# Kernel optimization log

Measured on AMD Instinct MI355X. Metric: run time of the kernel, lower is better.

## Reference

```python
import jax, jax.numpy as jnp
import numpy as np

NUM_HEADS = 16  # init kwarg num_attention_heads


def setup_inputs() -> dict:
    key = jax.random.key(0)
    k1, k2, k3, k4 = jax.random.split(key, 4)
    B, T, E = 2, 2048, 1024
    query = jax.random.normal(k1, (B, T, E), dtype=jnp.float32)
    key_t = jax.random.normal(k2, (B, T, E), dtype=jnp.float32)
    value = jax.random.normal(k3, (B, T, E), dtype=jnp.float32)
    # final output projection (nn.Linear(hidden, hidden, bias=False)); torch stores [out,in]
    W_out = jax.random.normal(k4, (E, E), dtype=jnp.float32) * 0.02
    return {"query": query, "key": key_t, "value": value, "W_out": W_out}


def reference(query, key, value, W_out):
    # NOTE: in the source, the per-head q_i/k_i/v_i linear projections are
    # overwritten by reshapes of the raw inputs, so the qs/ks/vs weights are
    # dead code. Every head computes identical output; mean over heads is a
    # no-op. We reproduce that exact math here.
    B, T, E = query.shape
    H = NUM_HEADS
    d = E // H  # head_dim; also d_k used in the 1/sqrt(d_k) scaling

    def split_heads(x):  # [B,T,E] -> [B,H,T,d]
        return x.reshape(B, T, H, d).transpose(0, 2, 1, 3)

    q = split_heads(query)
    k = split_heads(key)
    v = split_heads(value)

    scale = jnp.sqrt(jnp.asarray(d, dtype=jnp.float32))
    scores = jnp.einsum('bhtd,bhsd->bhts', q, k) / scale  # [B,H,T,T]
    attn = jax.nn.softmax(scores, axis=-1)
    head = jnp.einsum('bhts,bhsd->bhtd', attn, v)         # [B,H,T,d]
    head = head.transpose(0, 2, 1, 3).reshape(B, T, E)    # concat heads

    # mean over H identical head outputs == head; final linear (no bias)
    outputs = head @ W_out.T                              # [B,T,E]
    # mean over H identical attention maps == attn, returned as [B*H,T,T]
    attention = attn.reshape(B * H, T, T)
    return outputs, attention
```

## Files before the change

kernel.cpp:

```cpp
#include <hip/hip_runtime.h>
#include <hip/hip_fp16.h>

#define B_NUM  2
#define T_DIM  2048
#define E_DIM  1024
#define H_NUM  16
#define D_HEAD 64
#define BH_NUM (B_NUM * H_NUM)
#define NT     (T_DIM / 64)

using half8  = __attribute__((ext_vector_type(8))) _Float16;
using half4v = __attribute__((ext_vector_type(4))) _Float16;
using f32x4  = __attribute__((ext_vector_type(4))) float;

#define AS1 __attribute__((address_space(1)))
#define AS3 __attribute__((address_space(3)))

#define QSCALE 0.18033688011112042f

#define BAR_VM(N)                                                       \
    do {                                                                \
        asm volatile("s_waitcnt vmcnt(" #N ")" ::: "memory");           \
        __builtin_amdgcn_s_barrier();                                   \
        __builtin_amdgcn_sched_barrier(0);                              \
    } while (0)

__device__ __forceinline__ void bar_plain() {
    __builtin_amdgcn_s_barrier();
    __builtin_amdgcn_sched_barrier(0);
}

__global__ void cast_f16_kernel(const float* __restrict__ in,
                                _Float16* __restrict__ out, int n4) {
    int stride = gridDim.x * blockDim.x;
    for (int i = blockIdx.x * blockDim.x + threadIdx.x; i < n4; i += stride) {
        float4 v = reinterpret_cast<const float4*>(in)[i];
        half4v h;
        h[0] = (_Float16)v.x; h[1] = (_Float16)v.y;
        h[2] = (_Float16)v.z; h[3] = (_Float16)v.w;
        reinterpret_cast<half4v*>(out)[i] = h;
    }
}

__global__ void transpose_v_kernel(const float* __restrict__ V,
                                   _Float16* __restrict__ Vt) {
    __shared__ float tile[64][65];
    int s0 = blockIdx.x * 64;
    int bh = blockIdx.y;
    int b = bh >> 4, h = bh & 15;
    int t = threadIdx.x;

    int row = t >> 2;
    int c0  = (t & 3) * 16;
    const float* src = V + ((size_t)(b * T_DIM + s0 + row)) * E_DIM + h * D_HEAD + c0;
#pragma unroll
    for (int j = 0; j < 16; j += 4) {
        float4 v = *reinterpret_cast<const float4*>(src + j);
        tile[row][c0 + j + 0] = v.x;
        tile[row][c0 + j + 1] = v.y;
        tile[row][c0 + j + 2] = v.z;
        tile[row][c0 + j + 3] = v.w;
    }
    __syncthreads();

    int d  = t >> 2;
    int sc = (t & 3) * 16;
    half8 h0, h1;
#pragma unroll
    for (int j = 0; j < 8; ++j) {
        h0[j] = (_Float16)tile[sc + j][d];
        h1[j] = (_Float16)tile[sc + 8 + j][d];
    }
    _Float16* dst = Vt + ((size_t)(bh * D_HEAD + d)) * T_DIM + s0 + sc;
    *reinterpret_cast<half8*>(dst)     = h0;
    *reinterpret_cast<half8*>(dst + 8) = h1;
}

__device__ __forceinline__ void stage_gl(const _Float16* __restrict__ g,
                                         size_t stride, _Float16* lds,
                                         int w, int lane) {
    int r0 = lane >> 3;
    int c  = (lane & 7) ^ r0;
#pragma unroll
    for (int j = 0; j < 2; ++j) {
        int r = (w + 4 * j) * 8 + r0;
        const _Float16* src = g + (size_t)r * stride + c * 8;
        _Float16* dst = lds + (w + 4 * j) * 512;
        __builtin_amdgcn_global_load_lds((const AS1 void*)src, (AS3 void*)dst,
                                         16, 0, 0);
    }
}

__device__ __forceinline__ half8 read_frag64(const _Float16* lds, int row, int chunk) {
    int csw = chunk ^ (row & 7);
    return *reinterpret_cast<const half8*>(lds + row * 64 + csw * 8);
}

__global__ __launch_bounds__(256) void attn_kernel(
        const float* __restrict__ Q, const _Float16* __restrict__ Kh,
        const _Float16* __restrict__ Vt, float* __restrict__ attn_out,
        _Float16* __restrict__ head_h) {
    __shared__ __align__(16) _Float16 kbuf[2][64 * 64];
    __shared__ __align__(16) _Float16 vbuf[2][64 * 64];
    __shared__ __align__(16) _Float16 pbuf[4][16 * 64];

    int tid  = threadIdx.x;
    int wq   = tid >> 6;
    int lane = tid & 63;
    int l15  = lane & 15;
    int lg   = lane >> 4;

    int flat = blockIdx.x;
    int i    = flat >> 3;
    int bh   = (flat & 7) * 4 + (i >> 4);
    int q0   = (i & 15) * 128;
    int b = bh >> 4, h = bh & 15;

    half8 qfA[2], qfB[2];
#pragma unroll
    for (int half_ = 0; half_ < 2; ++half_) {
        const float* qsrc = Q + ((size_t)(b * T_DIM + q0 + half_ * 64 + wq * 16 + l15)) * E_DIM
                          + h * D_HEAD;
        half8* qf = half_ ? qfB : qfA;
#pragma unroll
        for (int ks = 0; ks < 2; ++ks) {
            float4 a0 = *reinterpret_cast<const float4*>(qsrc + (lg + 4 * ks) * 8);
            float4 a1 = *reinterpret_cast<const float4*>(qsrc + (lg + 4 * ks) * 8 + 4);
            qf[ks][0] = (_Float16)(a0.x * QSCALE); qf[ks][1] = (_Float16)(a0.y * QSCALE);
            qf[ks][2] = (_Float16)(a0.z * QSCALE); qf[ks][3] = (_Float16)(a0.w * QSCALE);
            qf[ks][4] = (_Float16)(a1.x * QSCALE); qf[ks][5] = (_Float16)(a1.y * QSCALE);
            qf[ks][6] = (_Float16)(a1.z * QSCALE); qf[ks][7] = (_Float16)(a1.w * QSCALE);
        }
    }

    const _Float16* kg = Kh + ((size_t)b * T_DIM) * E_DIM + h * D_HEAD;
    const _Float16* vg = Vt + (size_t)bh * D_HEAD * T_DIM;

#define P1TILE(KB, QF, LS)                                                     \
    {                                                                          \
        f32x4 acc[4];                                                          \
        _Pragma("unroll")                                                      \
        for (int ct = 0; ct < 4; ++ct) acc[ct] = (f32x4){0.f, 0.f, 0.f, 0.f};  \
        _Pragma("unroll")                                                      \
        for (int ks = 0; ks < 2; ++ks)                                         \
            _Pragma("unroll")                                                  \
            for (int ct = 0; ct < 4; ++ct) {                                   \
                half8 kf = read_frag64((KB), ct * 16 + l15, lg + 4 * ks);      \
                acc[ct] = __builtin_amdgcn_mfma_f32_16x16x32_f16(              \
                    kf, (QF)[ks], acc[ct], 0, 0, 0);                           \
            }                                                                  \
        _Pragma("unroll")                                                      \
        for (int ct = 0; ct < 4; ++ct)                                         \
            _Pragma("unroll")                                                  \
            for (int r = 0; r < 4; ++r)                                        \
                (LS) += __builtin_amdgcn_exp2f(acc[ct][r]);                    \
    }

#define P2TILE(KB, VB, QF, RL, ABROW, OACC)                                    \
    {                                                                          \
        f32x4 acc[4];                                                          \
        _Pragma("unroll")                                                      \
        for (int ct = 0; ct < 4; ++ct) acc[ct] = (f32x4){0.f, 0.f, 0.f, 0.f};  \
        _Pragma("unroll")                                                      \
        for (int ks = 0; ks < 2; ++ks)                                         \
            _Pragma("unroll")                                                  \
            for (int ct = 0; ct < 4; ++ct) {                                   \
                half8 kf = read_frag64((KB), ct * 16 + l15, lg + 4 * ks);      \
                acc[ct] = __builtin_amdgcn_mfma_f32_16x16x32_f16(              \
                    kf, (QF)[ks], acc[ct], 0, 0, 0);                           \
            }                                                                  \
        _Pragma("unroll")                                                      \
        for (int ct = 0; ct < 4; ++ct) {                                       \
            f32x4 p;                                                           \
            p[0] = __builtin_amdgcn_exp2f(acc[ct][0]) * (RL);                  \
            p[1] = __builtin_amdgcn_exp2f(acc[ct][1]) * (RL);                  \
            p[2] = __builtin_amdgcn_exp2f(acc[ct][2]) * (RL);                  \
            p[3] = __builtin_amdgcn_exp2f(acc[ct][3]) * (RL);                  \
            *reinterpret_cast<f32x4*>((ABROW) + ct * 16) = p;                  \
            half4v ph;                                                         \
            ph[0] = (_Float16)p[0]; ph[1] = (_Float16)p[1];                    \
            ph[2] = (_Float16)p[2]; ph[3] = (_Float16)p[3];                    \
            int cc = (ct * 4 + lg) ^ l15;                                      \
            *reinterpret_cast<half4v*>(pw + l15 * 64 + cc * 4) = ph;           \
        }                                                                      \
    }

#define PVTILE(VB, OACC)                                                       \
    {                                                                          \
        _Pragma("unroll")                                                      \
        for (int ks = 0; ks < 2; ++ks) {                                       \
            int c0 = 2 * (lg + 4 * ks);                                        \
            half4v lo = *reinterpret_cast<const half4v*>(                      \
                pw + l15 * 64 + ((c0)     ^ l15) * 4);                         \
            half4v hi = *reinterpret_cast<const half4v*>(                      \
                pw + l15 * 64 + ((c0 + 1) ^ l15) * 4);                         \
            half8 pa;                                                          \
            pa[0] = lo[0]; pa[1] = lo[1]; pa[2] = lo[2]; pa[3] = lo[3];        \
            pa[4] = hi[0]; pa[5] = hi[1]; pa[6] = hi[2]; pa[7] = hi[3];        \
            _Pragma("unroll")                                                  \
            for (int cd = 0; cd < 4; ++cd) {                                   \
                half8 vf = read_frag64((VB), cd * 16 + l15, lg + 4 * ks);      \
                (OACC)[cd] = __builtin_amdgcn_mfma_f32_16x16x32_f16(           \
                    pa, vf, (OACC)[cd], 0, 0, 0);                              \
            }                                                                  \
        }                                                                      \
    }

    float* ab = attn_out + (size_t)bh * T_DIM * T_DIM;
    _Float16* pw = pbuf[wq];
    int myqA = q0 + wq * 16 + l15;
    int myqB = myqA + 64;

    float lsumA = 0.0f, lsumB = 0.0f;
    int cur = 0;
    stage_gl(kg, E_DIM, kbuf[0], wq, lane);
    for (int t = 0; t < NT - 1; ++t) {
        stage_gl(kg + (size_t)(t + 1) * 64 * E_DIM, E_DIM, kbuf[cur ^ 1], wq, lane);
        BAR_VM(2);
        P1TILE(kbuf[cur], qfA, lsumA);
        bar_plain();
        cur ^= 1;
    }
    BAR_VM(0);
    P1TILE(kbuf[cur], qfA, lsumA);

    lsumA += __shfl_xor(lsumA, 16);
    lsumA += __shfl_xor(lsumA, 32);
    float rlA = 1.0f / lsumA;

    f32x4 oacc[4];
#pragma unroll
    for (int cd = 0; cd < 4; ++cd) oacc[cd] = (f32x4){0.f, 0.f, 0.f, 0.f};

    bar_plain();

    cur = 0;
    stage_gl(kg, E_DIM, kbuf[0], wq, lane);
    stage_gl(vg, T_DIM, vbuf[0], wq, lane);
    for (int t = 0; t < NT; ++t) {
        if (t < NT - 1) {
            stage_gl(kg + (size_t)(t + 1) * 64 * E_DIM, E_DIM, kbuf[cur ^ 1], wq, lane);
            stage_gl(vg + (t + 1) * 64, T_DIM, vbuf[cur ^ 1], wq, lane);
        }
        if (t == 0)           BAR_VM(4);
        else if (t < NT - 1)  BAR_VM(8);
        else                  BAR_VM(4);
        const _Float16* kb = kbuf[cur];
        const _Float16* vb = vbuf[cur];

        float* abrowA = ab + (size_t)myqA * T_DIM + t * 64 + lg * 4;
        P2TILE(kb, vb, qfA, rlA, abrowA, oacc);
        P1TILE(kb, qfB, lsumB);
        PVTILE(vb, oacc);
        bar_plain();
        cur ^= 1;
    }

    lsumB += __shfl_xor(lsumB, 16);
    lsumB += __shfl_xor(lsumB, 32);
    float rlB = 1.0f / lsumB;

    {
        _Float16* hw = head_h + ((size_t)(b * T_DIM + q0 + wq * 16)) * E_DIM + h * D_HEAD;
#pragma unroll
        for (int cd = 0; cd < 4; ++cd)
#pragma unroll
            for (int r = 0; r < 4; ++r)
                hw[(size_t)(lg * 4 + r) * E_DIM + cd * 16 + l15] = (_Float16)oacc[cd][r];
    }

#pragma unroll
    for (int cd = 0; cd < 4; ++cd) oacc[cd] = (f32x4){0.f, 0.f, 0.f, 0.f};

    cur = 0;
    stage_gl(kg, E_DIM, kbuf[0], wq, lane);
    stage_gl(vg, T_DIM, vbuf[0], wq, lane);
    for (int t = 0; t < NT; ++t) {
        if (t < NT - 1) {
            stage_gl(kg + (size_t)(t + 1) * 64 * E_DIM, E_DIM, kbuf[cur ^ 1], wq, lane);
            stage_gl(vg + (t + 1) * 64, T_DIM, vbuf[cur ^ 1], wq, lane);
        }
        if (t == 0)           BAR_VM(4);
        else if (t < NT - 1)  BAR_VM(8);
        else                  BAR_VM(4);
        const _Float16* kb = kbuf[cur];
        const _Float16* vb = vbuf[cur];

        float* abrowB = ab + (size_t)myqB * T_DIM + t * 64 + lg * 4;
        P2TILE(kb, vb, qfB, rlB, abrowB, oacc);
        PVTILE(vb, oacc);
        bar_plain();
        cur ^= 1;
    }

    {
        _Float16* hw = head_h + ((size_t)(b * T_DIM + q0 + 64 + wq * 16)) * E_DIM + h * D_HEAD;
#pragma unroll
        for (int cd = 0; cd < 4; ++cd)
#pragma unroll
            for (int r = 0; r < 4; ++r)
                hw[(size_t)(lg * 4 + r) * E_DIM + cd * 16 + l15] = (_Float16)oacc[cd][r];
    }
#undef P1TILE
#undef P2TILE
#undef PVTILE
}

__global__ __launch_bounds__(256) void proj_kernel(
        const _Float16* __restrict__ A, const _Float16* __restrict__ Wh,
        float* __restrict__ out) {
    __shared__ __align__(16) _Float16 abuf[2][64 * 64];
    __shared__ __align__(16) _Float16 bbuf[2][64 * 64];

    int tid  = threadIdx.x;
    int wq   = tid >> 6;
    int lane = tid & 63;
    int l15  = lane & 15;
    int lg   = lane >> 4;

    int m0 = blockIdx.x * 64;
    int n0 = blockIdx.y * 64;

    f32x4 acc[4];
#pragma unroll
    for (int ct = 0; ct < 4; ++ct) acc[ct] = (f32x4){0.f, 0.f, 0.f, 0.f};

    int cur = 0;
    stage_gl(A  + (size_t)m0 * E_DIM, E_DIM, abuf[0], wq, lane);
    stage_gl(Wh + (size_t)n0 * E_DIM, E_DIM, bbuf[0], wq, lane);
    for (int t = 0; t < E_DIM / 64; ++t) {
        if (t + 1 < E_DIM / 64) {
            stage_gl(A  + (size_t)m0 * E_DIM + (t + 1) * 64, E_DIM, abuf[cur ^ 1], wq, lane);
            stage_gl(Wh + (size_t)n0 * E_DIM + (t + 1) * 64, E_DIM, bbuf[cur ^ 1], wq, lane);
            BAR_VM(4);
        } else {
            BAR_VM(0);
        }
#pragma unroll
        for (int ks = 0; ks < 2; ++ks) {
            half8 hf = read_frag64(abuf[cur], wq * 16 + l15, lg + 4 * ks);
#pragma unroll
            for (int ct = 0; ct < 4; ++ct) {
                half8 wf = read_frag64(bbuf[cur], ct * 16 + l15, lg + 4 * ks);
                acc[ct] = __builtin_amdgcn_mfma_f32_16x16x32_f16(wf, hf, acc[ct], 0, 0, 0);
            }
        }
        bar_plain();
        cur ^= 1;
    }

    float* orow = out + (size_t)(m0 + wq * 16 + l15) * E_DIM + n0 + lg * 4;
#pragma unroll
    for (int ct = 0; ct < 4; ++ct) {
        f32x4 o;
        o[0] = acc[ct][0]; o[1] = acc[ct][1]; o[2] = acc[ct][2]; o[3] = acc[ct][3];
        *reinterpret_cast<f32x4*>(orow + ct * 16) = o;
    }
}

extern "C" void kernel_launch(void* const* d_in, const int* in_sizes, int n_in,
                              void* d_out, int out_size, void* d_ws, size_t ws_size,
                              hipStream_t stream) {
    const float* q = (const float*)d_in[0];
    const float* k = (const float*)d_in[1];
    const float* v = (const float*)d_in[2];
    const float* w = (const float*)d_in[3];

    float* outs = (float*)d_out;
    float* attn = outs + (size_t)B_NUM * T_DIM * E_DIM;

    char* ws = (char*)d_ws;
    _Float16* Kh = (_Float16*)(ws);
    _Float16* Vt = (_Float16*)(ws + (size_t)(8  << 20));
    _Float16* Wh = (_Float16*)(ws + (size_t)(16 << 20));
    _Float16* Hh = (_Float16*)(ws + (size_t)(18 << 20));

    int nqkv4 = B_NUM * T_DIM * E_DIM / 4;
    int nw4   = E_DIM * E_DIM / 4;

    cast_f16_kernel<<<1024, 256, 0, stream>>>(k, Kh, nqkv4);
    cast_f16_kernel<<<512, 256, 0, stream>>>(w, Wh, nw4);
    transpose_v_kernel<<<dim3(T_DIM / 64, BH_NUM), 256, 0, stream>>>(v, Vt);
    attn_kernel<<<(T_DIM / 128) * BH_NUM, 256, 0, stream>>>(q, Kh, Vt, attn, Hh);
    proj_kernel<<<dim3((B_NUM * T_DIM) / 64, E_DIM / 64), 256, 0, stream>>>(Hh, Wh, outs);
}
```

Before: 228.0 us.

## Fuse prep kernels, rotate KV tile order, add MFMA priority and deeper pass-1 prefetch

Merges the K cast, W cast and V transpose into one prep kernel launch to save launch overhead and tail gaps. In the attention kernel, each block starts its KV sweep at a rotated tile offset so that blocks sharing a head hit different K/V tiles at the same moment. The first (row-sum) pass now prefetches two tiles at a time, borrowing vbuf as a second double buffer. The MFMA sections are wrapped in s_setprio to favour matrix issue. Together these aim to cut launch count, cache and channel contention and pipeline stalls, at the cost of more complex indexing.

After: 203.9 us. 1.12x faster.

```diff
diff --git a/kernel.cpp b/kernel.cpp
--- a/kernel.cpp
+++ b/kernel.cpp
@@ -30,50 +30,60 @@
     __builtin_amdgcn_sched_barrier(0);
 }
 
-__global__ void cast_f16_kernel(const float* __restrict__ in,
-                                _Float16* __restrict__ out, int n4) {
-    int stride = gridDim.x * blockDim.x;
-    for (int i = blockIdx.x * blockDim.x + threadIdx.x; i < n4; i += stride) {
-        float4 v = reinterpret_cast<const float4*>(in)[i];
-        half4v h;
-        h[0] = (_Float16)v.x; h[1] = (_Float16)v.y;
-        h[2] = (_Float16)v.z; h[3] = (_Float16)v.w;
-        reinterpret_cast<half4v*>(out)[i] = h;
-    }
-}
-
-__global__ void transpose_v_kernel(const float* __restrict__ V,
-                                   _Float16* __restrict__ Vt) {
+#define TP_BLOCKS  (NT * BH_NUM)
+#define CAST_BLOCKS 1280
+__global__ void prep_kernel(const float* __restrict__ kin,
+                            const float* __restrict__ win,
+                            const float* __restrict__ V,
+                            _Float16* __restrict__ Kh,
+                            _Float16* __restrict__ Wh,
+                            _Float16* __restrict__ Vt,
+                            int nk4, int ntot4) {
     __shared__ float tile[64][65];
-    int s0 = blockIdx.x * 64;
-    int bh = blockIdx.y;
-    int b = bh >> 4, h = bh & 15;
     int t = threadIdx.x;
 
-    int row = t >> 2;
-    int c0  = (t & 3) * 16;
-    const float* src = V + ((size_t)(b * T_DIM + s0 + row)) * E_DIM + h * D_HEAD + c0;
-#pragma unroll
-    for (int j = 0; j < 16; j += 4) {
-        float4 v = *reinterpret_cast<const float4*>(src + j);
-        tile[row][c0 + j + 0] = v.x;
-        tile[row][c0 + j + 1] = v.y;
-        tile[row][c0 + j + 2] = v.z;
-        tile[row][c0 + j + 3] = v.w;
-    }
-    __syncthreads();
-
-    int d  = t >> 2;
-    int sc = (t & 3) * 16;
-    half8 h0, h1;
-#pragma unroll
-    for (int j = 0; j < 8; ++j) {
-        h0[j] = (_Float16)tile[sc + j][d];
-        h1[j] = (_Float16)tile[sc + 8 + j][d];
-    }
-    _Float16* dst = Vt + ((size_t)(bh * D_HEAD + d)) * T_DIM + s0 + sc;
-    *reinterpret_cast<half8*>(dst)     = h0;
-    *reinterpret_cast<half8*>(dst + 8) = h1;
+    if (blockIdx.x < TP_BLOCKS) {
+        int s0 = (blockIdx.x & 31) * 64;
+        int bh = blockIdx.x >> 5;
+        int b = bh >> 4, h = bh & 15;
+
+        int row = t >> 2;
+        int c0  = (t & 3) * 16;
+        const float* src = V + ((size_t)(b * T_DIM + s0 + row)) * E_DIM + h * D_HEAD + c0;
+#pragma unroll
+        for (int j = 0; j < 16; j += 4) {
+            float4 v = *reinterpret_cast<const float4*>(src + j);
+            tile[row][c0 + j + 0] = v.x;
+            tile[row][c0 + j + 1] = v.y;
+            tile[row][c0 + j + 2] = v.z;
+            tile[row][c0 + j + 3] = v.w;
+        }
+        __syncthreads();
+
+        int d  = t >> 2;
+        int sc = (t & 3) * 16;
+        half8 h0, h1;
+#pragma unroll
+        for (int j = 0; j < 8; ++j) {
+            h0[j] = (_Float16)tile[sc + j][d];
+            h1[j] = (_Float16)tile[sc + 8 + j][d];
+        }
+        _Float16* dst = Vt + ((size_t)(bh * D_HEAD + d)) * T_DIM + s0 + sc;
+        *reinterpret_cast<half8*>(dst)     = h0;
+        *reinterpret_cast<half8*>(dst + 8) = h1;
+    } else {
+        int stride = CAST_BLOCKS * 256;
+        for (int i = (blockIdx.x - TP_BLOCKS) * 256 + t; i < ntot4; i += stride) {
+            const float* src = (i < nk4) ? kin : win;
+            _Float16* dst    = (i < nk4) ? Kh  : Wh;
+            int j            = (i < nk4) ? i   : i - nk4;
+            float4 v = reinterpret_cast<const float4*>(src)[j];
+            half4v hh;
+            hh[0] = (_Float16)v.x; hh[1] = (_Float16)v.y;
+            hh[2] = (_Float16)v.z; hh[3] = (_Float16)v.w;
+            reinterpret_cast<half4v*>(dst)[j] = hh;
+        }
+    }
 }
 
 __device__ __forceinline__ void stage_gl(const _Float16* __restrict__ g,
@@ -94,6 +104,18 @@
 __device__ __forceinline__ half8 read_frag64(const _Float16* lds, int row, int chunk) {
     int csw = chunk ^ (row & 7);
     return *reinterpret_cast<const half8*>(lds + row * 64 + csw * 8);
+}
+
+__device__ __forceinline__ void load_qfrag(const float* qsrc, int lg, half8* qf) {
+#pragma unroll
+    for (int ks = 0; ks < 2; ++ks) {
+        float4 a0 = *reinterpret_cast<const float4*>(qsrc + (lg + 4 * ks) * 8);
+        float4 a1 = *reinterpret_cast<const float4*>(qsrc + (lg + 4 * ks) * 8 + 4);
+        qf[ks][0] = (_Float16)(a0.x * QSCALE); qf[ks][1] = (_Float16)(a0.y * QSCALE);
+        qf[ks][2] = (_Float16)(a0.z * QSCALE); qf[ks][3] = (_Float16)(a0.w * QSCALE);
+        qf[ks][4] = (_Float16)(a1.x * QSCALE); qf[ks][5] = (_Float16)(a1.y * QSCALE);
+        qf[ks][6] = (_Float16)(a1.z * QSCALE); qf[ks][7] = (_Float16)(a1.w * QSCALE);
+    }
 }
 
 __global__ __launch_bounds__(256) void attn_kernel(
@@ -113,25 +135,15 @@
     int flat = blockIdx.x;
     int i    = flat >> 3;
     int bh   = (flat & 7) * 4 + (i >> 4);
-    int q0   = (i & 15) * 128;
+    int qt   = i & 15;
+    int q0   = qt * 128;
+    int rot  = i & 31;
+    int rot2 = rot & 30;
     int b = bh >> 4, h = bh & 15;
 
     half8 qfA[2], qfB[2];
-#pragma unroll
-    for (int half_ = 0; half_ < 2; ++half_) {
-        const float* qsrc = Q + ((size_t)(b * T_DIM + q0 + half_ * 64 + wq * 16 + l15)) * E_DIM
-                          + h * D_HEAD;
-        half8* qf = half_ ? qfB : qfA;
-#pragma unroll
-        for (int ks = 0; ks < 2; ++ks) {
-            float4 a0 = *reinterpret_cast<const float4*>(qsrc + (lg + 4 * ks) * 8);
-            float4 a1 = *reinterpret_cast<const float4*>(qsrc + (lg + 4 * ks) * 8 + 4);
-            qf[ks][0] = (_Float16)(a0.x * QSCALE); qf[ks][1] = (_Float16)(a0.y * QSCALE);
-            qf[ks][2] = (_Float16)(a0.z * QSCALE); qf[ks][3] = (_Float16)(a0.w * QSCALE);
-            qf[ks][4] = (_Float16)(a1.x * QSCALE); qf[ks][5] = (_Float16)(a1.y * QSCALE);
-            qf[ks][6] = (_Float16)(a1.z * QSCALE); qf[ks][7] = (_Float16)(a1.w * QSCALE);
-        }
-    }
+    load_qfrag(Q + ((size_t)(b * T_DIM + q0 + wq * 16 + l15)) * E_DIM + h * D_HEAD, lg, qfA);
+    load_qfrag(Q + ((size_t)(b * T_DIM + q0 + 64 + wq * 16 + l15)) * E_DIM + h * D_HEAD, lg, qfB);
 
     const _Float16* kg = Kh + ((size_t)b * T_DIM) * E_DIM + h * D_HEAD;
     const _Float16* vg = Vt + (size_t)bh * D_HEAD * T_DIM;
@@ -141,6 +153,7 @@
         f32x4 acc[4];                                                          \
         _Pragma("unroll")                                                      \
         for (int ct = 0; ct < 4; ++ct) acc[ct] = (f32x4){0.f, 0.f, 0.f, 0.f};  \
+        __builtin_amdgcn_s_setprio(1);                                         \
         _Pragma("unroll")                                                      \
         for (int ks = 0; ks < 2; ++ks)                                         \
             _Pragma("unroll")                                                  \
@@ -149,6 +162,7 @@
                 acc[ct] = __builtin_amdgcn_mfma_f32_16x16x32_f16(              \
                     kf, (QF)[ks], acc[ct], 0, 0, 0);                           \
             }                                                                  \
+        __builtin_amdgcn_s_setprio(0);                                         \
         _Pragma("unroll")                                                      \
         for (int ct = 0; ct < 4; ++ct)                                         \
             _Pragma("unroll")                                                  \
@@ -156,11 +170,12 @@
                 (LS) += __builtin_amdgcn_exp2f(acc[ct][r]);                    \
     }
 
-#define P2TILE(KB, VB, QF, RL, ABROW, OACC)                                    \
+#define P2HEAD(KB, QF, RL, ABROW)                                              \
     {                                                                          \
         f32x4 acc[4];                                                          \
         _Pragma("unroll")                                                      \
         for (int ct = 0; ct < 4; ++ct) acc[ct] = (f32x4){0.f, 0.f, 0.f, 0.f};  \
+        __builtin_amdgcn_s_setprio(1);                                         \
         _Pragma("unroll")                                                      \
         for (int ks = 0; ks < 2; ++ks)                                         \
             _Pragma("unroll")                                                  \
@@ -169,6 +184,7 @@
                 acc[ct] = __builtin_amdgcn_mfma_f32_16x16x32_f16(              \
                     kf, (QF)[ks], acc[ct], 0, 0, 0);                           \
             }                                                                  \
+        __builtin_amdgcn_s_setprio(0);                                         \
         _Pragma("unroll")                                                      \
         for (int ct = 0; ct < 4; ++ct) {                                       \
             f32x4 p;                                                           \
@@ -185,8 +201,9 @@
         }                                                                      \
     }
 
-#define PVTILE(VB, OACC)                                                       \
+#define PVTILE(VB)                                                             \
     {                                                                          \
+        __builtin_amdgcn_s_setprio(1);                                         \
         _Pragma("unroll")                                                      \
         for (int ks = 0; ks < 2; ++ks) {                                       \
             int c0 = 2 * (lg + 4 * ks);                                        \
@@ -200,10 +217,11 @@
             _Pragma("unroll")                                                  \
             for (int cd = 0; cd < 4; ++cd) {                                   \
                 half8 vf = read_frag64((VB), cd * 16 + l15, lg + 4 * ks);      \
-                (OACC)[cd] = __builtin_amdgcn_mfma_f32_16x16x32_f16(           \
-                    pa, vf, (OACC)[cd], 0, 0, 0);                              \
+                oacc[cd] = __builtin_amdgcn_mfma_f32_16x16x32_f16(             \
+                    pa, vf, oacc[cd], 0, 0, 0);                                \
             }                                                                  \
         }                                                                      \
+        __builtin_amdgcn_s_setprio(0);                                         \
     }
 
     float* ab = attn_out + (size_t)bh * T_DIM * T_DIM;
@@ -211,18 +229,33 @@
     int myqA = q0 + wq * 16 + l15;
     int myqB = myqA + 64;
 
+#define IDX1(n) (((n) + rot2) & 31)
     float lsumA = 0.0f, lsumB = 0.0f;
-    int cur = 0;
-    stage_gl(kg, E_DIM, kbuf[0], wq, lane);
-    for (int t = 0; t < NT - 1; ++t) {
-        stage_gl(kg + (size_t)(t + 1) * 64 * E_DIM, E_DIM, kbuf[cur ^ 1], wq, lane);
-        BAR_VM(2);
-        P1TILE(kbuf[cur], qfA, lsumA);
-        bar_plain();
-        cur ^= 1;
-    }
-    BAR_VM(0);
-    P1TILE(kbuf[cur], qfA, lsumA);
+    stage_gl(kg + (size_t)IDX1(0) * 64 * E_DIM, E_DIM, kbuf[0], wq, lane);
+    stage_gl(kg + (size_t)IDX1(1) * 64 * E_DIM, E_DIM, kbuf[1], wq, lane);
+    for (int tt = 0; tt < NT / 2; tt += 2) {
+        {
+            stage_gl(kg + (size_t)IDX1(2 * tt + 2) * 64 * E_DIM, E_DIM, vbuf[0], wq, lane);
+            stage_gl(kg + (size_t)IDX1(2 * tt + 3) * 64 * E_DIM, E_DIM, vbuf[1], wq, lane);
+            BAR_VM(4);
+            P1TILE(kbuf[0], qfA, lsumA);
+            P1TILE(kbuf[1], qfA, lsumA);
+            bar_plain();
+        }
+        {
+            if (tt + 2 < NT / 2) {
+                stage_gl(kg + (size_t)IDX1(2 * tt + 4) * 64 * E_DIM, E_DIM, kbuf[0], wq, lane);
+                stage_gl(kg + (size_t)IDX1(2 * tt + 5) * 64 * E_DIM, E_DIM, kbuf[1], wq, lane);
+                BAR_VM(4);
+            } else {
+                BAR_VM(0);
+            }
+            P1TILE(vbuf[0], qfA, lsumA);
+            P1TILE(vbuf[1], qfA, lsumA);
+            bar_plain();
+        }
+    }
+#undef IDX1
 
     lsumA += __shfl_xor(lsumA, 16);
     lsumA += __shfl_xor(lsumA, 32);
@@ -234,13 +267,18 @@
 
     bar_plain();
 
-    cur = 0;
-    stage_gl(kg, E_DIM, kbuf[0], wq, lane);
-    stage_gl(vg, T_DIM, vbuf[0], wq, lane);
+    int cur = 0;
+    {
+        int p0 = rot;
+        stage_gl(kg + (size_t)p0 * 64 * E_DIM, E_DIM, kbuf[0], wq, lane);
+        stage_gl(vg + p0 * 64, T_DIM, vbuf[0], wq, lane);
+    }
     for (int t = 0; t < NT; ++t) {
+        int phys = (t + rot) & 31;
         if (t < NT - 1) {
-            stage_gl(kg + (size_t)(t + 1) * 64 * E_DIM, E_DIM, kbuf[cur ^ 1], wq, lane);
-            stage_gl(vg + (t + 1) * 64, T_DIM, vbuf[cur ^ 1], wq, lane);
+            int pn = (t + 1 + rot) & 31;
+            stage_gl(kg + (size_t)pn * 64 * E_DIM, E_DIM, kbuf[cur ^ 1], wq, lane);
+            stage_gl(vg + pn * 64, T_DIM, vbuf[cur ^ 1], wq, lane);
         }
         if (t == 0)           BAR_VM(4);
         else if (t < NT - 1)  BAR_VM(8);
@@ -248,10 +286,10 @@
         const _Float16* kb = kbuf[cur];
         const _Float16* vb = vbuf[cur];
 
-        float* abrowA = ab + (size_t)myqA * T_DIM + t * 64 + lg * 4;
-        P2TILE(kb, vb, qfA, rlA, abrowA, oacc);
+        float* abrowA = ab + (size_t)myqA * T_DIM + phys * 64 + lg * 4;
+        P2HEAD(kb, qfA, rlA, abrowA);
         P1TILE(kb, qfB, lsumB);
-        PVTILE(vb, oacc);
+        PVTILE(vb);
         bar_plain();
         cur ^= 1;
     }
@@ -273,12 +311,17 @@
     for (int cd = 0; cd < 4; ++cd) oacc[cd] = (f32x4){0.f, 0.f, 0.f, 0.f};
 
     cur = 0;
-    stage_gl(kg, E_DIM, kbuf[0], wq, lane);
-    stage_gl(vg, T_DIM, vbuf[0], wq, lane);
+    {
+        int p0 = rot;
+        stage_gl(kg + (size_t)p0 * 64 * E_DIM, E_DIM, kbuf[0], wq, lane);
+        stage_gl(vg + p0 * 64, T_DIM, vbuf[0], wq, lane);
+    }
     for (int t = 0; t < NT; ++t) {
+        int phys = (t + rot) & 31;
         if (t < NT - 1) {
-            stage_gl(kg + (size_t)(t + 1) * 64 * E_DIM, E_DIM, kbuf[cur ^ 1], wq, lane);
-            stage_gl(vg + (t + 1) * 64, T_DIM, vbuf[cur ^ 1], wq, lane);
+            int pn = (t + 1 + rot) & 31;
+            stage_gl(kg + (size_t)pn * 64 * E_DIM, E_DIM, kbuf[cur ^ 1], wq, lane);
+            stage_gl(vg + pn * 64, T_DIM, vbuf[cur ^ 1], wq, lane);
         }
         if (t == 0)           BAR_VM(4);
         else if (t < NT - 1)  BAR_VM(8);
@@ -286,9 +329,9 @@
         const _Float16* kb = kbuf[cur];
         const _Float16* vb = vbuf[cur];
 
-        float* abrowB = ab + (size_t)myqB * T_DIM + t * 64 + lg * 4;
-        P2TILE(kb, vb, qfB, rlB, abrowB, oacc);
-        PVTILE(vb, oacc);
+        float* abrowB = ab + (size_t)myqB * T_DIM + phys * 64 + lg * 4;
+        P2HEAD(kb, qfB, rlB, abrowB);
+        PVTILE(vb);
         bar_plain();
         cur ^= 1;
     }
@@ -302,7 +345,7 @@
                 hw[(size_t)(lg * 4 + r) * E_DIM + cd * 16 + l15] = (_Float16)oacc[cd][r];
     }
 #undef P1TILE
-#undef P2TILE
+#undef P2HEAD
 #undef PVTILE
 }
 
@@ -375,12 +418,11 @@
     _Float16* Wh = (_Float16*)(ws + (size_t)(16 << 20));
     _Float16* Hh = (_Float16*)(ws + (size_t)(18 << 20));
 
-    int nqkv4 = B_NUM * T_DIM * E_DIM / 4;
-    int nw4   = E_DIM * E_DIM / 4;
-
-    cast_f16_kernel<<<1024, 256, 0, stream>>>(k, Kh, nqkv4);
-    cast_f16_kernel<<<512, 256, 0, stream>>>(w, Wh, nw4);
-    transpose_v_kernel<<<dim3(T_DIM / 64, BH_NUM), 256, 0, stream>>>(v, Vt);
+    int nk4 = B_NUM * T_DIM * E_DIM / 4;
+    int nw4 = E_DIM * E_DIM / 4;
+
+    prep_kernel<<<TP_BLOCKS + CAST_BLOCKS, 256, 0, stream>>>(
+        k, w, v, Kh, Wh, Vt, nk4, nk4 + nw4);
     attn_kernel<<<(T_DIM / 128) * BH_NUM, 256, 0, stream>>>(q, Kh, Vt, attn, Hh);
     proj_kernel<<<dim3((B_NUM * T_DIM) / 64, E_DIM / 64), 256, 0, stream>>>(Hh, Wh, outs);
 }
```
